# Kernel tuning notes

Measured on AMD Instinct MI355X. Metric: run time of the kernel, lower is better.

The kernel has to match this reference:

```python
import jax, jax.numpy as jnp
import numpy as np

HEADS, HID, OUT_C, IN_C = 8, 128, 2, 64
D = HID // HEADS
NODE = {"cell0": 50000, "cell1": 100000, "cell2": 25000}
# (src_type, dst_type, edge_name, num_edges)
ETYPES = [("cell0", "cell0", "u00", 200000),
          ("cell1", "cell1", "u11", 200000),
          ("cell1", "cell0", "b10", 100000),
          ("cell2", "cell1", "b21", 50000)]


def _segment_softmax(scores, seg, num_segments):
    # numerically-stable softmax over irregular destination segments
    m = jax.ops.segment_max(scores, seg, num_segments=num_segments)
    e = jnp.exp(scores - m[seg])
    s = jax.ops.segment_sum(e, seg, num_segments=num_segments)
    return e / (s[seg] + 1e-16)


def setup_inputs() -> dict:
    key = jax.random.key(0)
    ks = iter(jax.random.split(key, 64))
    s = 0.1
    inp = {}
    for nt, n in NODE.items():
        inp[f"x_{nt}"] = jax.random.normal(next(ks), (n, IN_C), jnp.float32)
    for st, dt, name, e in ETYPES:
        src = jax.random.randint(next(ks), (e,), 0, NODE[st], jnp.int32)
        dst = jax.random.randint(next(ks), (e,), 0, NODE[dt], jnp.int32)
        inp[f"ei_{name}"] = jnp.stack([src, dst])
    # HANConv params: per node-type projection, per edge-type attention vectors
    for nt in NODE:
        inp[f"W_{nt}"] = jax.random.normal(next(ks), (IN_C, HID), jnp.float32) * s
        inp[f"b_{nt}"] = jnp.zeros((HID,), jnp.float32)
    for _, _, name, _ in ETYPES:
        inp[f"as_{name}"] = jax.random.normal(next(ks), (HEADS, D), jnp.float32) * s
        inp[f"ad_{name}"] = jax.random.normal(next(ks), (HEADS, D), jnp.float32) * s
    # semantic attention params + final classifier
    inp["k_w"] = jax.random.normal(next(ks), (HID, HID), jnp.float32) * s
    inp["k_b"] = jnp.zeros((HID,), jnp.float32)
    inp["q"] = jax.random.normal(next(ks), (HID,), jnp.float32) * s
    inp["lin_w"] = jax.random.normal(next(ks), (HID, OUT_C), jnp.float32) * s
    inp["lin_b"] = jnp.zeros((OUT_C,), jnp.float32)
    return inp


def _han_conv(x, ei, W, b, att_s, att_d, k_w, k_b, q):
    # node-level: project each node type -> [N, H, D]
    h = {nt: (x[nt] @ W[nt] + b[nt]).reshape(-1, HEADS, D) for nt in NODE}
    outs = {nt: [] for nt in NODE}
    for st, dt, name, _ in ETYPES:
        xs, xd = h[st], h[dt]
        a_s = (xs * att_s[name]).sum(-1)  # [Ns, H]
        a_d = (xd * att_d[name]).sum(-1)  # [Nd, H]
        src, dst = ei[name][0], ei[name][1]
        alpha = jax.nn.leaky_relu(a_s[src] + a_d[dst], 0.2)  # [E, H]
        alpha = _segment_softmax(alpha, dst, NODE[dt])
        msg = xs[src] * alpha[:, :, None]  # [E, H, D]
        agg = jax.ops.segment_sum(msg, dst, num_segments=NODE[dt])
        outs[dt].append(jax.nn.relu(agg.reshape(-1, HID)))
    # semantic-level attention across metapaths per dst node type
    res = {}
    for nt, lst in outs.items():
        if not lst:
            res[nt] = None
            continue
        stk = jnp.stack(lst)  # [M, N, HID]
        score = (q * jnp.tanh(stk @ k_w + k_b).mean(1)).sum(-1)  # [M]
        attn = jax.nn.softmax(score)
        res[nt] = jnp.einsum('m,mnf->nf', attn, stk)
    return res


def reference(x_cell0, x_cell1, x_cell2,
              W_cell0, b_cell0, W_cell1, b_cell1, W_cell2, b_cell2,
              as_u00, ad_u00, as_u11, ad_u11, as_b10, ad_b10, as_b21, ad_b21,
              k_w, k_b, q, lin_w, lin_b,
              ei_u00, ei_u11, ei_b10, ei_b21):
    x = {"cell0": x_cell0, "cell1": x_cell1, "cell2": x_cell2}
    ei = {"u00": ei_u00, "u11": ei_u11, "b10": ei_b10, "b21": ei_b21}
    W = {"cell0": W_cell0, "cell1": W_cell1, "cell2": W_cell2}
    b = {"cell0": b_cell0, "cell1": b_cell1, "cell2": b_cell2}
    att_s = {"u00": as_u00, "u11": as_u11, "b10": as_b10, "b21": as_b21}
    att_d = {"u00": ad_u00, "u11": ad_u11, "b10": ad_b10, "b21": ad_b21}
    # HAN.forward calls han_conv twice with identical inputs (first result
    # discarded); in eval mode (dropout off) both calls are identical math,
    # so we compute it once.
    out = _han_conv(x, ei, W, b, att_s, att_d, k_w, k_b, q)
    pooled = sum(jnp.sum(v, axis=0) for v in out.values() if v is not None)  # global_add_pool, batch=None
    return jax.nn.sigmoid(pooled[None, :] @ lin_w + lin_b)  # [1, OUT_C]
```

## Files before the change

kernel.cpp:

```cpp
#include <hip/hip_runtime.h>
#include <hip/hip_fp16.h>

#define N0 50000
#define N1 100000
#define N2 25000
#define E00 200000
#define E11 200000
#define E10 100000
#define E21 50000
#define EE  550000
#define ND  300000
#define NB  293
#define NT_ALL 18750
#define HID 128
#define INC 64

typedef _Float16 half8 __attribute__((ext_vector_type(8)));
typedef float float4v __attribute__((ext_vector_type(4)));
typedef float floatx2 __attribute__((ext_vector_type(2)));

struct PT {
    const float* x; const float* W; const float* bias; unsigned char* h;
    const float* av0; const float* av1; const float* av2; const float* av3;
    float* ao0; float* ao1; float* ao2; float* ao3;
    int N; int ntiles; int bstart; int nblocks;
};

#define WPAD 72
#define HPAD 136

__global__ __launch_bounds__(256) void proj_mfma(PT t0, PT t1, PT t2)
{
    __shared__ _Float16 WT[128 * WPAD];
    __shared__ _Float16 AdT[32 * WPAD];
    __shared__ _Float16 ht[4][16][HPAD];
    const int tid = threadIdx.x;
    const int lane = tid & 63, wv = tid >> 6;
    const int fi = lane & 15, hi = lane >> 4;

    PT A = (blockIdx.x >= t2.bstart) ? t2 : (blockIdx.x >= t1.bstart) ? t1 : t0;

    for (int idx = tid; idx < 64 * 128; idx += 256) {
        int g = idx >> 7, f = idx & 127;
        WT[f * WPAD + g] = (_Float16)A.W[idx];
    }
    __syncthreads();
    const float* avs[4] = {A.av0, A.av1, A.av2, A.av3};
    for (int idx = tid; idx < 32 * 64; idx += 256) {
        int c = idx & 31, g = idx >> 5;
        const float* av = avs[c >> 3];
        float v = 0.f;
        if (av) {
            int hh = c & 7;
#pragma unroll
            for (int d = 0; d < 16; ++d)
                v += (float)WT[(hh * 16 + d) * WPAD + g] * av[hh * 16 + d];
        }
        AdT[c * WPAD + g] = (_Float16)v;
    }
    __syncthreads();

    half8 bfr[8][2], bd[2][2];
#pragma unroll
    for (int nt = 0; nt < 8; ++nt)
#pragma unroll
        for (int kb = 0; kb < 2; ++kb)
            bfr[nt][kb] = *(const half8*)&WT[(nt * 16 + fi) * WPAD + kb * 32 + hi * 8];
#pragma unroll
    for (int t = 0; t < 2; ++t)
#pragma unroll
        for (int kb = 0; kb < 2; ++kb)
            bd[t][kb] = *(const half8*)&AdT[(t * 16 + fi) * WPAD + kb * 32 + hi * 8];

    float bvv[8];
#pragma unroll
    for (int nt = 0; nt < 8; ++nt) bvv[nt] = A.bias[nt * 16 + fi];
    float bdc[2] = {0.f, 0.f};
    {
        int hh = fi & 7;
        const float* alo = (fi >= 8) ? A.av1 : A.av0;
        const float* ahi = (fi >= 8) ? A.av3 : A.av2;
#pragma unroll
        for (int d = 0; d < 16; ++d) {
            float bb = A.bias[hh * 16 + d];
            if (alo) bdc[0] += bb * alo[hh * 16 + d];
            if (ahi) bdc[1] += bb * ahi[hh * 16 + d];
        }
    }
    float* aolo = (fi >= 8) ? A.ao1 : A.ao0;
    float* aohi = (fi >= 8) ? A.ao3 : A.ao2;
    const bool has_hi = (A.av2 != nullptr) || (A.av3 != nullptr);

    const int stride = A.nblocks * 4;
    for (int t = (blockIdx.x - A.bstart) * 4 + wv; t < A.ntiles; t += stride) {
        const int base = t * 16;
        int rsrc = base + fi; if (rsrc >= A.N) rsrc = A.N - 1;
        const float* xp = A.x + (size_t)rsrc * 64 + hi * 8;
        float4 u0 = *(const float4*)(xp);
        float4 u1 = *(const float4*)(xp + 4);
        float4 u2 = *(const float4*)(xp + 32);
        float4 u3 = *(const float4*)(xp + 36);
        half8 a0, a1;
        a0[0] = (_Float16)u0.x; a0[1] = (_Float16)u0.y; a0[2] = (_Float16)u0.z; a0[3] = (_Float16)u0.w;
        a0[4] = (_Float16)u1.x; a0[5] = (_Float16)u1.y; a0[6] = (_Float16)u1.z; a0[7] = (_Float16)u1.w;
        a1[0] = (_Float16)u2.x; a1[1] = (_Float16)u2.y; a1[2] = (_Float16)u2.z; a1[3] = (_Float16)u2.w;
        a1[4] = (_Float16)u3.x; a1[5] = (_Float16)u3.y; a1[6] = (_Float16)u3.z; a1[7] = (_Float16)u3.w;

        float4v c[8];
#pragma unroll
        for (int nt = 0; nt < 8; ++nt) {
            float4v z = {0.f, 0.f, 0.f, 0.f};
            z = __builtin_amdgcn_mfma_f32_16x16x32_f16(a0, bfr[nt][0], z, 0, 0, 0);
            z = __builtin_amdgcn_mfma_f32_16x16x32_f16(a1, bfr[nt][1], z, 0, 0, 0);
            c[nt] = z;
        }
        float4v d0 = {0.f, 0.f, 0.f, 0.f};
        d0 = __builtin_amdgcn_mfma_f32_16x16x32_f16(a0, bd[0][0], d0, 0, 0, 0);
        d0 = __builtin_amdgcn_mfma_f32_16x16x32_f16(a1, bd[0][1], d0, 0, 0, 0);
        float4v d1 = {0.f, 0.f, 0.f, 0.f};
        if (has_hi) {
            d1 = __builtin_amdgcn_mfma_f32_16x16x32_f16(a0, bd[1][0], d1, 0, 0, 0);
            d1 = __builtin_amdgcn_mfma_f32_16x16x32_f16(a1, bd[1][1], d1, 0, 0, 0);
        }

#pragma unroll
        for (int nt = 0; nt < 8; ++nt)
#pragma unroll
            for (int r = 0; r < 4; ++r)
                ht[wv][hi * 4 + r][nt * 16 + fi] = (_Float16)(c[nt][r] + bvv[nt]);
#pragma unroll
        for (int i = 0; i < 4; ++i) {
            int row = i * 4 + hi;
            int node = base + row;
            if (node < A.N) {
                half8 v = *(const half8*)&ht[wv][row][fi * 8];
                int pa = __builtin_amdgcn_cvt_pk_fp8_f32((float)v[0], (float)v[1], 0, false);
                pa = __builtin_amdgcn_cvt_pk_fp8_f32((float)v[2], (float)v[3], pa, true);
                int pb = __builtin_amdgcn_cvt_pk_fp8_f32((float)v[4], (float)v[5], 0, false);
                pb = __builtin_amdgcn_cvt_pk_fp8_f32((float)v[6], (float)v[7], pb, true);
                int2 o = {pa, pb};
                *(int2*)(A.h + (size_t)node * 128 + fi * 8) = o;
            }
        }
        if (aolo) {
#pragma unroll
            for (int r = 0; r < 4; ++r) {
                int node = base + hi * 4 + r;
                if (node < A.N) aolo[(size_t)node * 8 + (fi & 7)] = d0[r] + bdc[0];
            }
        }
        if (aohi) {
#pragma unroll
            for (int r = 0; r < 4; ++r) {
                int node = base + hi * 4 + r;
                if (node < A.N) aohi[(size_t)node * 8 + (fi & 7)] = d1[r] + bdc[1];
            }
        }
    }
}

__device__ __forceinline__ void decode_edge(
    int e, const int* ei00, const int* ei10, const int* ei11, const int* ei21,
    int& src, int& slot)
{
    if (e < E00)                    { src = ei00[e];               slot = ei00[E00 + e]; }
    else if (e < E00 + E10)         { int i = e - E00;             src = ei10[i]; slot = 50000  + ei10[E10 + i]; }
    else if (e < E00 + E10 + E11)   { int i = e - E00 - E10;       src = ei11[i]; slot = 100000 + ei11[E11 + i]; }
    else                            { int i = e - E00 - E10 - E11; src = ei21[i]; slot = 200000 + ei21[E21 + i]; }
}

__global__ __launch_bounds__(256) void count_kernel(
    const int* __restrict__ ei00, const int* __restrict__ ei10,
    const int* __restrict__ ei11, const int* __restrict__ ei21,
    int* __restrict__ cnt)
{
    int e = blockIdx.x * 256 + threadIdx.x;
    if (e >= EE) return;
    int src, slot;
    decode_edge(e, ei00, ei10, ei11, ei21, src, slot);
    atomicAdd(&cnt[slot], 1);
}

__global__ __launch_bounds__(256) void scan1_kernel(
    const int* __restrict__ cnt, int* __restrict__ part)
{
    const int tid = threadIdx.x, b = blockIdx.x;
    int i0 = b * 1024 + tid * 4;
    int s = 0;
#pragma unroll
    for (int k = 0; k < 4; ++k) { int i = i0 + k; s += (i < ND) ? cnt[i] : 0; }
#pragma unroll
    for (int off = 1; off < 64; off <<= 1) s += __shfl_xor(s, off);
    __shared__ int wt[4];
    if ((tid & 63) == 0) wt[tid >> 6] = s;
    __syncthreads();
    if (tid == 0) part[b] = wt[0] + wt[1] + wt[2] + wt[3];
}

__global__ __launch_bounds__(256) void scan2_kernel(int* __restrict__ part)
{
    const int t = threadIdx.x;
    int p0 = (2 * t     < NB) ? part[2 * t]     : 0;
    int p1 = (2 * t + 1 < NB) ? part[2 * t + 1] : 0;
    int ps = p0 + p1;
    __shared__ int sd[256];
    sd[t] = ps; __syncthreads();
    for (int d = 1; d < 256; d <<= 1) {
        int v = (t >= d) ? sd[t - d] : 0;
        __syncthreads();
        sd[t] += v;
        __syncthreads();
    }
    int exc = sd[t] - ps;
    if (2 * t     < NB) part[2 * t]     = exc;
    if (2 * t + 1 < NB) part[2 * t + 1] = exc + p0;
}

__global__ __launch_bounds__(256) void scan3_kernel(
    const int* __restrict__ cnt, const int* __restrict__ part,
    int* __restrict__ off, int* __restrict__ cursor)
{
    const int tid = threadIdx.x, b = blockIdx.x;
    const int lane = tid & 63, wv = tid >> 6;
    int i0 = b * 1024 + tid * 4;
    int v[4];
#pragma unroll
    for (int k = 0; k < 4; ++k) { int i = i0 + k; v[k] = (i < ND) ? cnt[i] : 0; }
    int ts = v[0] + v[1] + v[2] + v[3];
    int inc = ts;
#pragma unroll
    for (int d = 1; d < 64; d <<= 1) {
        int u = __shfl_up(inc, d);
        if (lane >= d) inc += u;
    }
    int wexc = inc - ts;
    __shared__ int wt[4];
    if (lane == 63) wt[wv] = inc;
    __syncthreads();
    int wbase = 0;
    for (int w = 0; w < wv; ++w) wbase += wt[w];
    int base = part[b] + wbase + wexc;
    int pre = 0;
#pragma unroll
    for (int k = 0; k < 4; ++k) {
        int i = i0 + k;
        if (i < ND) { off[i] = base + pre; cursor[i] = base + pre; }
        pre += v[k];
    }
}

__global__ __launch_bounds__(256) void fill_kernel(
    const int* __restrict__ ei00, const int* __restrict__ ei10,
    const int* __restrict__ ei11, const int* __restrict__ ei21,
    const float* __restrict__ as00, const float* __restrict__ ad00,
    const float* __restrict__ as10, const float* __restrict__ ad10,
    const float* __restrict__ as11, const float* __restrict__ ad11,
    const float* __restrict__ as21, const float* __restrict__ ad21,
    int* __restrict__ cursor, int* __restrict__ srcs, _Float16* __restrict__ wgt)
{
    int e = blockIdx.x * 256 + threadIdx.x;
    if (e >= EE) return;
    int src, d, slot;
    const float* asp; const float* adp;
    if (e < E00) {
        src = ei00[e]; d = ei00[E00 + e]; slot = d; asp = as00; adp = ad00;
    } else if (e < E00 + E10) {
        int i = e - E00; src = ei10[i]; d = ei10[E10 + i]; slot = 50000 + d; asp = as10; adp = ad10;
    } else if (e < E00 + E10 + E11) {
        int i = e - E00 - E10; src = ei11[i]; d = ei11[E11 + i]; slot = 100000 + d; asp = as11; adp = ad11;
    } else {
        int i = e - E00 - E10 - E11; src = ei21[i]; d = ei21[E21 + i]; slot = 200000 + d; asp = as21; adp = ad21;
    }
    float4 sa0 = *(const float4*)(asp + (size_t)src * 8);
    float4 sa1 = *(const float4*)(asp + (size_t)src * 8 + 4);
    float4 da0 = *(const float4*)(adp + (size_t)d * 8);
    float4 da1 = *(const float4*)(adp + (size_t)d * 8 + 4);
    float vv[8] = {sa0.x + da0.x, sa0.y + da0.y, sa0.z + da0.z, sa0.w + da0.w,
                   sa1.x + da1.x, sa1.y + da1.y, sa1.z + da1.z, sa1.w + da1.w};
    half8 w;
#pragma unroll
    for (int h = 0; h < 8; ++h) {
        float v = vv[h];
        v = v > 0.f ? v : 0.2f * v;
        w[h] = (_Float16)__expf(v);
    }
    int pos = atomicAdd(&cursor[slot], 1);
    srcs[pos] = src;
    *(half8*)(wgt + (size_t)pos * 8) = w;
}

__global__ __launch_bounds__(256) void gather_kernel(
    const int* __restrict__ cnt, const int* __restrict__ off,
    const int* __restrict__ srcs, const _Float16* __restrict__ wgt,
    const unsigned char* __restrict__ h0, const unsigned char* __restrict__ h1,
    const unsigned char* __restrict__ h2,
    unsigned char* __restrict__ agg)
{
    const int gid = blockIdx.x * 256 + threadIdx.x;
    const int lane = gid & 63;
    const int grp = lane >> 4, lg = lane & 15;
    const int slot = (gid >> 6) * 4 + grp;
    const int head = lg >> 1;
    const unsigned char* hs = (slot < 50000) ? h0 : (slot < 200000) ? h1 : h2;
    const int deg = cnt[slot], st = off[slot];

    int degm = deg;
    degm = max(degm, __shfl_xor(degm, 16));
    degm = max(degm, __shfl_xor(degm, 32));

    float acc[8] = {0.f, 0.f, 0.f, 0.f, 0.f, 0.f, 0.f, 0.f};
    float sw = 0.f;
    int i = 0;
    for (; i + 2 <= degm; i += 2) {
        bool a0 = (i < deg), a1 = (i + 1 < deg);
        int s0 = 0, s1 = 0;
        if (a0) s0 = srcs[st + i];
        if (a1) s1 = srcs[st + i + 1];
        float w0 = 0.f, w1 = 0.f;
        unsigned long long v0 = 0, v1 = 0;
        if (a0) { w0 = (float)wgt[(size_t)(st + i) * 8 + head];
                  v0 = *(const unsigned long long*)(hs + (size_t)s0 * 128 + lg * 8); }
        if (a1) { w1 = (float)wgt[(size_t)(st + i + 1) * 8 + head];
                  v1 = *(const unsigned long long*)(hs + (size_t)s1 * 128 + lg * 8); }
        int l0 = (int)(v0 & 0xffffffffu), m0 = (int)(v0 >> 32);
        int l1 = (int)(v1 & 0xffffffffu), m1 = (int)(v1 >> 32);
        floatx2 f0a = __builtin_amdgcn_cvt_pk_f32_fp8(l0, false);
        floatx2 f0b = __builtin_amdgcn_cvt_pk_f32_fp8(l0, true);
        floatx2 f0c = __builtin_amdgcn_cvt_pk_f32_fp8(m0, false);
        floatx2 f0d = __builtin_amdgcn_cvt_pk_f32_fp8(m0, true);
        floatx2 f1a = __builtin_amdgcn_cvt_pk_f32_fp8(l1, false);
        floatx2 f1b = __builtin_amdgcn_cvt_pk_f32_fp8(l1, true);
        floatx2 f1c = __builtin_amdgcn_cvt_pk_f32_fp8(m1, false);
        floatx2 f1d = __builtin_amdgcn_cvt_pk_f32_fp8(m1, true);
        acc[0] += w0 * f0a.x + w1 * f1a.x;
        acc[1] += w0 * f0a.y + w1 * f1a.y;
        acc[2] += w0 * f0b.x + w1 * f1b.x;
        acc[3] += w0 * f0b.y + w1 * f1b.y;
        acc[4] += w0 * f0c.x + w1 * f1c.x;
        acc[5] += w0 * f0c.y + w1 * f1c.y;
        acc[6] += w0 * f0d.x + w1 * f1d.x;
        acc[7] += w0 * f0d.y + w1 * f1d.y;
        sw += w0 + w1;
    }
    if (i < degm) {
        bool a0 = (i < deg);
        int s0 = 0;
        if (a0) s0 = srcs[st + i];
        float w0 = 0.f;
        unsigned long long v0 = 0;
        if (a0) { w0 = (float)wgt[(size_t)(st + i) * 8 + head];
                  v0 = *(const unsigned long long*)(hs + (size_t)s0 * 128 + lg * 8); }
        int l0 = (int)(v0 & 0xffffffffu), m0 = (int)(v0 >> 32);
        floatx2 f0a = __builtin_amdgcn_cvt_pk_f32_fp8(l0, false);
        floatx2 f0b = __builtin_amdgcn_cvt_pk_f32_fp8(l0, true);
        floatx2 f0c = __builtin_amdgcn_cvt_pk_f32_fp8(m0, false);
        floatx2 f0d = __builtin_amdgcn_cvt_pk_f32_fp8(m0, true);
        acc[0] += w0 * f0a.x; acc[1] += w0 * f0a.y;
        acc[2] += w0 * f0b.x; acc[3] += w0 * f0b.y;
        acc[4] += w0 * f0c.x; acc[5] += w0 * f0c.y;
        acc[6] += w0 * f0d.x; acc[7] += w0 * f0d.y;
        sw += w0;
    }

    float rr = __builtin_amdgcn_rcpf(sw + 1e-16f);
    float r[8];
#pragma unroll
    for (int j = 0; j < 8; ++j) r[j] = fmaxf(acc[j] * rr, 0.f);
    int pa = __builtin_amdgcn_cvt_pk_fp8_f32(r[0], r[1], 0, false);
    pa = __builtin_amdgcn_cvt_pk_fp8_f32(r[2], r[3], pa, true);
    int pb = __builtin_amdgcn_cvt_pk_fp8_f32(r[4], r[5], 0, false);
    pb = __builtin_amdgcn_cvt_pk_fp8_f32(r[6], r[7], pb, true);
    int2 o = {pa, pb};
    *(int2*)(agg + (size_t)slot * 128 + lg * 8) = o;
}

#define KSTRB 136
__global__ __launch_bounds__(256, 2) void semantic_kernel(
    const unsigned char* __restrict__ agg,
    const float* __restrict__ kw, const float* __restrict__ lw,
    const float* __restrict__ kb, const float* __restrict__ q,
    float* __restrict__ cs2, float* __restrict__ score)
{
    __shared__ unsigned char kwT[144 * KSTRB];
    __shared__ float redv[12];
    const int tid = threadIdx.x;
    const int lane = tid & 63, wv = tid >> 6;
    const int fi = lane & 15, hi = lane >> 4;

    for (int idx = tid; idx < 128 * 128; idx += 256) {
        int g = idx >> 7, f = idx & 127;
        int r = __builtin_amdgcn_cvt_pk_fp8_f32(kw[idx], 0.f, 0, false);
        kwT[f * KSTRB + g] = (unsigned char)r;
    }
    for (int idx = tid; idx < 16 * 128; idx += 256) {
        int f2 = idx >> 7, g = idx & 127;
        float v = (f2 < 2) ? lw[g * 2 + f2] : 0.f;
        int r = __builtin_amdgcn_cvt_pk_fp8_f32(v, 0.f, 0, false);
        kwT[(128 + f2) * KSTRB + g] = (unsigned char)r;
    }
    if (tid < 12) redv[tid] = 0.f;
    __syncthreads();

    long bf[9][4];
#pragma unroll
    for (int ft = 0; ft < 9; ++ft)
#pragma unroll
        for (int kk = 0; kk < 4; ++kk)
            bf[ft][kk] = *(const long*)&kwT[(ft * 16 + fi) * KSTRB + kk * 32 + hi * 8];

    float qv[8], kbv[8];
#pragma unroll
    for (int ft = 0; ft < 8; ++ft) {
        qv[ft] = q[ft * 16 + fi];
        kbv[ft] = kb[ft * 16 + fi];
    }

    float sc[4] = {0.f, 0.f, 0.f, 0.f};
    float cs[4] = {0.f, 0.f, 0.f, 0.f};
    const int nw = gridDim.x * 4;
    for (int t = blockIdx.x * 4 + wv; t < NT_ALL; t += nw) {
        const int m = (t >= 12500) ? 3 : (t >= 6250) ? 2 : (t >= 3125) ? 1 : 0;
        const unsigned char* rowp = agg + ((size_t)(t * 16 + fi) * 128 + hi * 8);
        long af[4];
        af[0] = *(const long*)(rowp);
        af[1] = *(const long*)(rowp + 32);
        af[2] = *(const long*)(rowp + 64);
        af[3] = *(const long*)(rowp + 96);
        float tsc = 0.f, tcs = 0.f;
#pragma unroll
        for (int ft = 0; ft < 8; ++ft) {
            float4v c = {0.f, 0.f, 0.f, 0.f};
            c = __builtin_amdgcn_mfma_f32_16x16x32_fp8_fp8(af[0], bf[ft][0], c, 0, 0, 0);
            c = __builtin_amdgcn_mfma_f32_16x16x32_fp8_fp8(af[1], bf[ft][1], c, 0, 0, 0);
            c = __builtin_amdgcn_mfma_f32_16x16x32_fp8_fp8(af[2], bf[ft][2], c, 0, 0, 0);
            c = __builtin_amdgcn_mfma_f32_16x16x32_fp8_fp8(af[3], bf[ft][3], c, 0, 0, 0);
#pragma unroll
            for (int r = 0; r < 4; ++r) {
                float y = c[r] + kbv[ft];
                float e = __expf(2.f * y);
                tsc += qv[ft] * (1.f - 2.f * __builtin_amdgcn_rcpf(e + 1.f));
            }
        }
        {
            float4v c = {0.f, 0.f, 0.f, 0.f};
            c = __builtin_amdgcn_mfma_f32_16x16x32_fp8_fp8(af[0], bf[8][0], c, 0, 0, 0);
            c = __builtin_amdgcn_mfma_f32_16x16x32_fp8_fp8(af[1], bf[8][1], c, 0, 0, 0);
            c = __builtin_amdgcn_mfma_f32_16x16x32_fp8_fp8(af[2], bf[8][2], c, 0, 0, 0);
            c = __builtin_amdgcn_mfma_f32_16x16x32_fp8_fp8(af[3], bf[8][3], c, 0, 0, 0);
            tcs = c[0] + c[1] + c[2] + c[3];
        }
        if (m == 0)      { sc[0] += tsc; cs[0] += tcs; }
        else if (m == 1) { sc[1] += tsc; cs[1] += tcs; }
        else if (m == 2) { sc[2] += tsc; cs[2] += tcs; }
        else             { sc[3] += tsc; cs[3] += tcs; }
    }

#pragma unroll
    for (int m = 0; m < 4; ++m) {
        float s = sc[m];
#pragma unroll
        for (int off = 1; off < 64; off <<= 1) s += __shfl_xor(s, off);
        if (lane == 0 && s != 0.f) atomicAdd(&redv[m], s);
        float v = cs[m];
        v += __shfl_xor(v, 16);
        v += __shfl_xor(v, 32);
        if (hi == 0 && fi < 2 && v != 0.f) atomicAdd(&redv[4 + 2 * m + fi], v);
    }
    __syncthreads();
    if (tid < 4)              atomicAdd(&score[tid], redv[tid]);
    if (tid >= 4 && tid < 12) atomicAdd(&cs2[tid - 4], redv[tid]);
}

__global__ void final_kernel(const float* __restrict__ cs2,
                             const float* __restrict__ score,
                             const float* __restrict__ lb,
                             float* __restrict__ out)
{
    float s0 = score[0] / (float)N0;
    float s1 = score[1] / (float)N0;
    float s2 = score[2] / (float)N1;
    float s3 = score[3] / (float)N1;
    float m0 = fmaxf(s0, s1);
    float e0 = expf(s0 - m0), e1 = expf(s1 - m0);
    float a0 = e0 / (e0 + e1), a1 = e1 / (e0 + e1);
    float m1 = fmaxf(s2, s3);
    float e2 = expf(s2 - m1), e3 = expf(s3 - m1);
    float a2 = e2 / (e2 + e3), a3 = e3 / (e2 + e3);
    float z0 = a0 * cs2[0] + a1 * cs2[2] + a2 * cs2[4] + a3 * cs2[6] + lb[0];
    float z1 = a0 * cs2[1] + a1 * cs2[3] + a2 * cs2[5] + a3 * cs2[7] + lb[1];
    out[0] = 1.f / (1.f + expf(-z0));
    out[1] = 1.f / (1.f + expf(-z1));
}

extern "C" void kernel_launch(void* const* d_in, const int* in_sizes, int n_in,
                              void* d_out, int out_size, void* d_ws, size_t ws_size,
                              hipStream_t stream)
{
    const float* x0  = (const float*)d_in[0];
    const float* x1  = (const float*)d_in[1];
    const float* x2  = (const float*)d_in[2];
    const int* ei00  = (const int*)d_in[3];
    const int* ei11  = (const int*)d_in[4];
    const int* ei10  = (const int*)d_in[5];
    const int* ei21  = (const int*)d_in[6];
    const float* W0  = (const float*)d_in[7];  const float* b0 = (const float*)d_in[8];
    const float* W1  = (const float*)d_in[9];  const float* b1 = (const float*)d_in[10];
    const float* W2  = (const float*)d_in[11]; const float* b2 = (const float*)d_in[12];
    const float* as00 = (const float*)d_in[13]; const float* ad00 = (const float*)d_in[14];
    const float* as11 = (const float*)d_in[15]; const float* ad11 = (const float*)d_in[16];
    const float* as10 = (const float*)d_in[17]; const float* ad10 = (const float*)d_in[18];
    const float* as21 = (const float*)d_in[19]; const float* ad21 = (const float*)d_in[20];
    const float* kw  = (const float*)d_in[21]; const float* kb  = (const float*)d_in[22];
    const float* q   = (const float*)d_in[23];
    const float* lw  = (const float*)d_in[24]; const float* lb  = (const float*)d_in[25];
    float* out = (float*)d_out;

    char* p = (char*)d_ws;
    auto alloc = [&](size_t bytes) {
        char* r = p;
        p += (bytes + 255) & ~(size_t)255;
        return r;
    };
    unsigned char* h0 = (unsigned char*)alloc((size_t)N0 * 128);
    unsigned char* h1 = (unsigned char*)alloc((size_t)N1 * 128);
    unsigned char* h2 = (unsigned char*)alloc((size_t)N2 * 128);
    float* o_as00 = (float*)alloc((size_t)N0 * 32);
    float* o_ad00 = (float*)alloc((size_t)N0 * 32);
    float* o_as11 = (float*)alloc((size_t)N1 * 32);
    float* o_ad11 = (float*)alloc((size_t)N1 * 32);
    float* o_as10 = (float*)alloc((size_t)N1 * 32);
    float* o_ad10 = (float*)alloc((size_t)N0 * 32);
    float* o_as21 = (float*)alloc((size_t)N2 * 32);
    float* o_ad21 = (float*)alloc((size_t)N1 * 32);
    int* off    = (int*)alloc((size_t)ND * 4);
    int* cursor = (int*)alloc((size_t)ND * 4);
    int* part   = (int*)alloc((size_t)512 * 4);
    int* srcs   = (int*)alloc((size_t)EE * 4);
    _Float16* wgt = (_Float16*)alloc((size_t)EE * 16);
    unsigned char* agg = (unsigned char*)alloc((size_t)ND * 128);
    char* zstart = p;
    int* cnt = (int*)alloc((size_t)ND * 4);
    float* colsum2 = (float*)alloc(8 * 4);
    float* score   = (float*)alloc(4 * 4);
    size_t zbytes = (size_t)(p - zstart);

    (void)hipMemsetAsync(zstart, 0, zbytes, stream);

    PT t0 = {x0, W0, b0, h0,
             as00, ad00, ad10, nullptr,
             o_as00, o_ad00, o_ad10, nullptr,
             N0, 3125, 0, 148};
    PT t1 = {x1, W1, b1, h1,
             as11, ad11, as10, ad21,
             o_as11, o_ad11, o_as10, o_ad21,
             N1, 6250, 148, 292};
    PT t2 = {x2, W2, b2, h2,
             as21, nullptr, nullptr, nullptr,
             o_as21, nullptr, nullptr, nullptr,
             N2, 1563, 440, 72};
    proj_mfma<<<512, 256, 0, stream>>>(t0, t1, t2);

    count_kernel<<<(EE + 255) / 256, 256, 0, stream>>>(ei00, ei10, ei11, ei21, cnt);
    scan1_kernel<<<NB, 256, 0, stream>>>(cnt, part);
    scan2_kernel<<<1, 256, 0, stream>>>(part);
    scan3_kernel<<<NB, 256, 0, stream>>>(cnt, part, off, cursor);
    fill_kernel<<<(EE + 255) / 256, 256, 0, stream>>>(ei00, ei10, ei11, ei21,
        o_as00, o_ad00, o_as10, o_ad10, o_as11, o_ad11, o_as21, o_ad21,
        cursor, srcs, wgt);

    gather_kernel<<<ND / 16, 256, 0, stream>>>(cnt, off, srcs, wgt, h0, h1, h2, agg);

    semantic_kernel<<<512, 256, 0, stream>>>(agg, kw, lw, kb, q, colsum2, score);

    final_kernel<<<1, 1, 0, stream>>>(colsum2, score, lb, out);
}
```

Baseline: 303.5 us.

## Split semantic kernel output tiles across waves to cut registers and raise occupancy

Each wave in the semantic kernel used to hold all nine column tiles of the fp8 weight matrix in registers and walk its own row tiles. Now the four waves of a block share one row tile, and each wave holds only two or three column tiles (the last wave also takes the classifier column). This lets the launch bound go from 2 to 4 blocks per CU and the grid grow from 512 to 1536 blocks. The aim is lower register pressure and more latency hiding. The cost is that every wave reloads the same row tile from global memory, so per-lane fetches quadruple (likely served from cache), and the last wave carries more work than the others.

Result: slower. 342.8 us (+12.9%).

```diff
diff --git a/kernel.cpp b/kernel.cpp
--- a/kernel.cpp
+++ b/kernel.cpp
@@ -375,7 +375,7 @@
 }
 
 #define KSTRB 136
-__global__ __launch_bounds__(256, 2) void semantic_kernel(
+__global__ __launch_bounds__(256, 4) void semantic_kernel(
     const unsigned char* __restrict__ agg,
     const float* __restrict__ kw, const float* __restrict__ lw,
     const float* __restrict__ kb, const float* __restrict__ q,
@@ -401,24 +401,29 @@
     if (tid < 12) redv[tid] = 0.f;
     __syncthreads();
 
-    long bf[9][4];
-#pragma unroll
-    for (int ft = 0; ft < 9; ++ft)
-#pragma unroll
-        for (int kk = 0; kk < 4; ++kk)
-            bf[ft][kk] = *(const long*)&kwT[(ft * 16 + fi) * KSTRB + kk * 32 + hi * 8];
-
-    float qv[8], kbv[8];
-#pragma unroll
-    for (int ft = 0; ft < 8; ++ft) {
-        qv[ft] = q[ft * 16 + fi];
-        kbv[ft] = kb[ft * 16 + fi];
+    const int ftbase = wv * 2;
+    const int nft = (wv == 3) ? 3 : 2;
+
+    long bf[3][4];
+    float qv[3], kbv[3];
+#pragma unroll
+    for (int i = 0; i < 3; ++i) {
+        if (i < nft) {
+            int ft = ftbase + i;
+#pragma unroll
+            for (int kk = 0; kk < 4; ++kk)
+                bf[i][kk] = *(const long*)&kwT[(ft * 16 + fi) * KSTRB + kk * 32 + hi * 8];
+            qv[i]  = (ft < 8) ? q[ft * 16 + fi]  : 0.f;
+            kbv[i] = (ft < 8) ? kb[ft * 16 + fi] : 0.f;
+        } else {
+            bf[i][0] = bf[i][1] = bf[i][2] = bf[i][3] = 0;
+            qv[i] = 0.f; kbv[i] = 0.f;
+        }
     }
 
     float sc[4] = {0.f, 0.f, 0.f, 0.f};
     float cs[4] = {0.f, 0.f, 0.f, 0.f};
-    const int nw = gridDim.x * 4;
-    for (int t = blockIdx.x * 4 + wv; t < NT_ALL; t += nw) {
+    for (int t = blockIdx.x; t < NT_ALL; t += gridDim.x) {
         const int m = (t >= 12500) ? 3 : (t >= 6250) ? 2 : (t >= 3125) ? 1 : 0;
         const unsigned char* rowp = agg + ((size_t)(t * 16 + fi) * 128 + hi * 8);
         long af[4];
@@ -428,26 +433,23 @@
         af[3] = *(const long*)(rowp + 96);
         float tsc = 0.f, tcs = 0.f;
 #pragma unroll
-        for (int ft = 0; ft < 8; ++ft) {
+        for (int i = 0; i < 3; ++i) {
+            if (i >= nft) continue;
             float4v c = {0.f, 0.f, 0.f, 0.f};
-            c = __builtin_amdgcn_mfma_f32_16x16x32_fp8_fp8(af[0], bf[ft][0], c, 0, 0, 0);
-            c = __builtin_amdgcn_mfma_f32_16x16x32_fp8_fp8(af[1], bf[ft][1], c, 0, 0, 0);
-            c = __builtin_amdgcn_mfma_f32_16x16x32_fp8_fp8(af[2], bf[ft][2], c, 0, 0, 0);
-            c = __builtin_amdgcn_mfma_f32_16x16x32_fp8_fp8(af[3], bf[ft][3], c, 0, 0, 0);
-#pragma unroll
-            for (int r = 0; r < 4; ++r) {
-                float y = c[r] + kbv[ft];
-                float e = __expf(2.f * y);
-                tsc += qv[ft] * (1.f - 2.f * __builtin_amdgcn_rcpf(e + 1.f));
+            c = __builtin_amdgcn_mfma_f32_16x16x32_fp8_fp8(af[0], bf[i][0], c, 0, 0, 0);
+            c = __builtin_amdgcn_mfma_f32_16x16x32_fp8_fp8(af[1], bf[i][1], c, 0, 0, 0);
+            c = __builtin_amdgcn_mfma_f32_16x16x32_fp8_fp8(af[2], bf[i][2], c, 0, 0, 0);
+            c = __builtin_amdgcn_mfma_f32_16x16x32_fp8_fp8(af[3], bf[i][3], c, 0, 0, 0);
+            if (ftbase + i == 8) {
+                tcs = c[0] + c[1] + c[2] + c[3];
+            } else {
+#pragma unroll
+                for (int r = 0; r < 4; ++r) {
+                    float y = c[r] + kbv[i];
+                    float e = __expf(2.f * y);
+                    tsc += qv[i] * (1.f - 2.f * __builtin_amdgcn_rcpf(e + 1.f));
+                }
             }
-        }
-        {
-            float4v c = {0.f, 0.f, 0.f, 0.f};
-            c = __builtin_amdgcn_mfma_f32_16x16x32_fp8_fp8(af[0], bf[8][0], c, 0, 0, 0);
-            c = __builtin_amdgcn_mfma_f32_16x16x32_fp8_fp8(af[1], bf[8][1], c, 0, 0, 0);
-            c = __builtin_amdgcn_mfma_f32_16x16x32_fp8_fp8(af[2], bf[8][2], c, 0, 0, 0);
-            c = __builtin_amdgcn_mfma_f32_16x16x32_fp8_fp8(af[3], bf[8][3], c, 0, 0, 0);
-            tcs = c[0] + c[1] + c[2] + c[3];
         }
         if (m == 0)      { sc[0] += tsc; cs[0] += tcs; }
         else if (m == 1) { sc[1] += tsc; cs[1] += tcs; }
@@ -570,7 +572,7 @@
 
     gather_kernel<<<ND / 16, 256, 0, stream>>>(cnt, off, srcs, wgt, h0, h1, h2, agg);
 
-    semantic_kernel<<<512, 256, 0, stream>>>(agg, kw, lw, kb, q, colsum2, score);
+    semantic_kernel<<<1536, 256, 0, stream>>>(agg, kw, lw, kb, q, colsum2, score);
 
     final_kernel<<<1, 1, 0, stream>>>(colsum2, score, lb, out);
 }
```
